# Optimization experiments

Hardware: AMD Instinct MI355X
Metric: run time of the kernel (lower is better)

The kernel has to match this reference:

```python
import jax, jax.numpy as jnp
import numpy as np

N_E = 4096
E_DIM = 256


def setup_inputs() -> dict:
    key = jax.random.key(0)
    k1, k2 = jax.random.split(key)
    z = jax.random.normal(k1, (32, 2048, E_DIM), dtype=jnp.float32)
    # nn.Embedding weight initialized uniform(-1/n_e, 1/n_e)
    codebook = jax.random.uniform(k2, (N_E, E_DIM), dtype=jnp.float32,
                                  minval=-1.0 / N_E, maxval=1.0 / N_E)
    return {"z": z, "codebook": codebook}


def reference(z, codebook):
    # z: [B, T, e_dim], codebook: [n_e, e_dim]
    z_flat = z.reshape(-1, z.shape[-1])                      # [N, d]
    # squared euclidean distance: ||z||^2 + ||e||^2 - 2 z.e^T
    d = (jnp.sum(z_flat ** 2, axis=1, keepdims=True)
         + jnp.sum(codebook ** 2, axis=1)
         - 2.0 * jnp.einsum('nd,kd->nk', z_flat, codebook))  # [N, n_e]
    idx = jnp.argmin(d, axis=1)                              # [N]
    z_q = codebook[idx].reshape(z.shape)                     # [B, T, d]
    return z_q
```

## Files before the change

### kernel.cpp

```cpp
#include <hip/hip_runtime.h>
#include <hip/hip_fp16.h>
#include <cfloat>
#include <climits>

#define D     256
#define NE    4096
#define MT    64
#define NSPLITB 8
#define DELTA     1.5e-4f
#define CAND_CAP  131072

typedef _Float16 f16x8 __attribute__((ext_vector_type(8)));
typedef __attribute__((ext_vector_type(4))) float f32x4;

#define SYNC(n) do { \
    asm volatile("s_waitcnt vmcnt(" #n ")\n\ts_barrier" ::: "memory"); \
    __builtin_amdgcn_sched_barrier(0); \
} while (0)

__device__ __forceinline__ float np_block128_sq(const float* __restrict__ p) {
    float r[8];
    #pragma unroll
    for (int j = 0; j < 8; ++j) r[j] = __fmul_rn(p[j], p[j]);
    #pragma unroll
    for (int i = 8; i < 128; i += 8)
        #pragma unroll
        for (int j = 0; j < 8; ++j) r[j] = __fadd_rn(r[j], __fmul_rn(p[i + j], p[i + j]));
    return __fadd_rn(__fadd_rn(__fadd_rn(r[0], r[1]), __fadd_rn(r[2], r[3])),
                     __fadd_rn(__fadd_rn(r[4], r[5]), __fadd_rn(r[6], r[7])));
}
__device__ __forceinline__ float np_sumsq256(const float* __restrict__ p) {
    return __fadd_rn(np_block128_sq(p), np_block128_sq(p + 128));
}
__device__ __forceinline__ float np_einsum_dot256(const float* __restrict__ zr,
                                                  const float* __restrict__ er) {
    float v0 = 0.f, v1 = 0.f, v2 = 0.f, v3 = 0.f;
    for (int t = 0; t < 256; t += 16) {
        float4 a0 = *(const float4*)(zr + t);
        float4 a1 = *(const float4*)(zr + t + 4);
        float4 a2 = *(const float4*)(zr + t + 8);
        float4 a3 = *(const float4*)(zr + t + 12);
        float4 b0 = *(const float4*)(er + t);
        float4 b1 = *(const float4*)(er + t + 4);
        float4 b2 = *(const float4*)(er + t + 8);
        float4 b3 = *(const float4*)(er + t + 12);
        v0 = __fadd_rn(v0, __fmul_rn(a3.x, b3.x));
        v1 = __fadd_rn(v1, __fmul_rn(a3.y, b3.y));
        v2 = __fadd_rn(v2, __fmul_rn(a3.z, b3.z));
        v3 = __fadd_rn(v3, __fmul_rn(a3.w, b3.w));
        v0 = __fadd_rn(v0, __fmul_rn(a2.x, b2.x));
        v1 = __fadd_rn(v1, __fmul_rn(a2.y, b2.y));
        v2 = __fadd_rn(v2, __fmul_rn(a2.z, b2.z));
        v3 = __fadd_rn(v3, __fmul_rn(a2.w, b2.w));
        v0 = __fadd_rn(v0, __fmul_rn(a1.x, b1.x));
        v1 = __fadd_rn(v1, __fmul_rn(a1.y, b1.y));
        v2 = __fadd_rn(v2, __fmul_rn(a1.z, b1.z));
        v3 = __fadd_rn(v3, __fmul_rn(a1.w, b1.w));
        v0 = __fadd_rn(v0, __fmul_rn(a0.x, b0.x));
        v1 = __fadd_rn(v1, __fmul_rn(a0.y, b0.y));
        v2 = __fadd_rn(v2, __fmul_rn(a0.z, b0.z));
        v3 = __fadd_rn(v3, __fmul_rn(a0.w, b0.w));
    }
    return __fadd_rn(__fadd_rn(v0, v1), __fadd_rn(v2, v3));
}

__global__ void bnp_kernel(const float* __restrict__ cb, float* __restrict__ Bnp) {
    int k = blockIdx.x * 256 + threadIdx.x;
    if (k < NE) Bnp[k] = np_sumsq256(cb + (size_t)k * D);
}

__global__ void cbhl_kernel(const float* __restrict__ cb,
                            unsigned short* __restrict__ hi,
                            unsigned short* __restrict__ lo) {
    int t = blockIdx.x * 256 + threadIdx.x;
    float4 v = *(const float4*)(cb + (size_t)t * 4);
    float e[4] = {v.x * 4096.f, v.y * 4096.f, v.z * 4096.f, v.w * 4096.f};
    ushort4 H, L;
    unsigned short* Hp = (unsigned short*)&H;
    unsigned short* Lp = (unsigned short*)&L;
    #pragma unroll
    for (int j = 0; j < 4; ++j) {
        _Float16 hh = (_Float16)e[j];
        _Float16 ll = (_Float16)((e[j] - (float)hh) * 2048.0f);
        Hp[j] = __builtin_bit_cast(unsigned short, hh);
        Lp[j] = __builtin_bit_cast(unsigned short, ll);
    }
    *(ushort4*)(hi + (size_t)t * 4) = H;
    *(ushort4*)(lo + (size_t)t * 4) = L;
}

__device__ __forceinline__ void gload_lds16(const void* g, void* l) {
    __builtin_amdgcn_global_load_lds(
        (const __attribute__((address_space(1))) unsigned int*)g,
        (__attribute__((address_space(3))) unsigned int*)l, 16, 0, 0);
}

__global__ __launch_bounds__(256, 3)
void stageA_f16(const float* __restrict__ z,
                const unsigned short* __restrict__ cb2,
                const float* __restrict__ Bnp, int* __restrict__ idxArr,
                float* __restrict__ rowMin, unsigned long long* __restrict__ rowKey,
                int* __restrict__ flagCnt, int* __restrict__ flagList) {
    __shared__ unsigned char lds[16384 + 4 * 8192];
    float* BnpL = (float*)lds;
    unsigned short* Bt = (unsigned short*)(lds + 16384);

    const int tid  = threadIdx.x;
    const int wid  = tid >> 6;
    const int lane = tid & 63;
    const int ln   = lane & 15;
    const int qd   = lane >> 4;
    const int wm   = wid & 1;
    const int wn   = wid >> 1;
    const int R0   = blockIdx.x * MT;

    #pragma unroll
    for (int i = 0; i < 4; ++i) {
        int j = tid + 256 * i;
        *(float4*)(BnpL + j * 4) = *(const float4*)(Bnp + j * 4);
    }

    f16x8 fa[8][2];
    {
        const float* za = z + (size_t)(R0 + wm * 32 + ln) * 256 + qd * 8;
        #pragma unroll
        for (int kc = 0; kc < 8; ++kc)
            #pragma unroll
            for (int mt = 0; mt < 2; ++mt) {
                const float* p = za + mt * 16 * 256 + kc * 32;
                float4 a = *(const float4*)p, b = *(const float4*)(p + 4);
                f16x8 h;
                h[0] = (_Float16)a.x; h[1] = (_Float16)a.y;
                h[2] = (_Float16)a.z; h[3] = (_Float16)a.w;
                h[4] = (_Float16)b.x; h[5] = (_Float16)b.y;
                h[6] = (_Float16)b.z; h[7] = (_Float16)b.w;
                fa[kc][mt] = h;
            }
    }

    const int cA  = wid * 32 + (lane >> 2);
    const int sgA = (lane & 3) ^ ((cA >> 1) & 3);
    const unsigned short* srcA = cb2 + cA * 256 + sgA * 8;
    unsigned short* dstW = Bt + wid * 1024;
    const int boffs = ((wn * 64 + ln) << 6) + ((qd ^ ((ln >> 1) & 3)) << 4);
    const unsigned char* btb = (const unsigned char*)Bt;

    float best1[8], best2[8];
    int   bidx[8];
    #pragma unroll
    for (int i = 0; i < 8; ++i) { best1[i] = FLT_MAX; best2[i] = FLT_MAX; bidx[i] = 0; }

    #pragma unroll
    for (int s = 0; s < 3; ++s) {
        gload_lds16(srcA + s * 32, dstW + s * 4096);
        gload_lds16(srcA + s * 32 + 4096, dstW + s * 4096 + 512);
    }
    __syncthreads();

    for (int ct = 0; ct < 31; ++ct) {
        f32x4 acc[2][4];
        #pragma unroll
        for (int i = 0; i < 2; ++i)
            #pragma unroll
            for (int j = 0; j < 4; ++j) acc[i][j] = (f32x4){0.f, 0.f, 0.f, 0.f};

        #pragma unroll
        for (int kc = 0; kc < 8; ++kc) {
            SYNC(4);
            {
                const int s3k = kc + 3;
                int off = (ct + (s3k >> 3)) * 32768 + (s3k & 7) * 32;
                unsigned short* d = dstW + ((s3k & 3) << 12);
                gload_lds16(srcA + off, d);
                gload_lds16(srcA + off + 4096, d + 512);
            }
            f16x8 fb[4];
            #pragma unroll
            for (int nt = 0; nt < 4; ++nt)
                fb[nt] = *(const f16x8*)(btb + ((kc & 3) << 13) + boffs + nt * 1024);
            __builtin_amdgcn_s_setprio(1);
            #pragma unroll
            for (int mt = 0; mt < 2; ++mt)
                #pragma unroll
                for (int nt = 0; nt < 4; ++nt)
                    acc[mt][nt] = __builtin_amdgcn_mfma_f32_16x16x32_f16(
                        fa[kc][mt], fb[nt], acc[mt][nt], 0, 0, 0);
            __builtin_amdgcn_s_setprio(0);

            if (kc == 7) {
                const int C0 = ct * 128;
                #pragma unroll
                for (int nt = 0; nt < 4; ++nt) {
                    int col = C0 + wn * 64 + nt * 16 + ln;
                    float bn = BnpL[col];
                    #pragma unroll
                    for (int mt = 0; mt < 2; ++mt) {
                        f32x4 a = acc[mt][nt];
                        #pragma unroll
                        for (int r = 0; r < 4; ++r) {
                            float s = fmaf(-4.8828125e-4f, a[r], bn);
                            int ii = mt * 4 + r;
                            bool lt = s < best1[ii];
                            best2[ii] = __builtin_amdgcn_fmed3f(best1[ii], best2[ii], s);
                            bidx[ii]  = lt ? col : bidx[ii];
                            best1[ii] = fminf(best1[ii], s);
                        }
                    }
                }
            }
        }
    }
    {
        const int ct = 31;
        f32x4 acc[2][4];
        #pragma unroll
        for (int i = 0; i < 2; ++i)
            #pragma unroll
            for (int j = 0; j < 4; ++j) acc[i][j] = (f32x4){0.f, 0.f, 0.f, 0.f};

        #pragma unroll
        for (int kc = 0; kc < 8; ++kc) {
            if (kc <= 5) { SYNC(4); } else if (kc == 6) { SYNC(2); } else { SYNC(0); }
            if (kc <= 4) {
                const int s3k = kc + 3;
                int off = ct * 32768 + (s3k & 7) * 32;
                unsigned short* d = dstW + ((s3k & 3) << 12);
                gload_lds16(srcA + off, d);
                gload_lds16(srcA + off + 4096, d + 512);
            }
            f16x8 fb[4];
            #pragma unroll
            for (int nt = 0; nt < 4; ++nt)
                fb[nt] = *(const f16x8*)(btb + ((kc & 3) << 13) + boffs + nt * 1024);
            __builtin_amdgcn_s_setprio(1);
            #pragma unroll
            for (int mt = 0; mt < 2; ++mt)
                #pragma unroll
                for (int nt = 0; nt < 4; ++nt)
                    acc[mt][nt] = __builtin_amdgcn_mfma_f32_16x16x32_f16(
                        fa[kc][mt], fb[nt], acc[mt][nt], 0, 0, 0);
            __builtin_amdgcn_s_setprio(0);

            if (kc == 7) {
                const int C0 = ct * 128;
                #pragma unroll
                for (int nt = 0; nt < 4; ++nt) {
                    int col = C0 + wn * 64 + nt * 16 + ln;
                    float bn = BnpL[col];
                    #pragma unroll
                    for (int mt = 0; mt < 2; ++mt) {
                        f32x4 a = acc[mt][nt];
                        #pragma unroll
                        for (int r = 0; r < 4; ++r) {
                            float s = fmaf(-4.8828125e-4f, a[r], bn);
                            int ii = mt * 4 + r;
                            bool lt = s < best1[ii];
                            best2[ii] = __builtin_amdgcn_fmed3f(best1[ii], best2[ii], s);
                            bidx[ii]  = lt ? col : bidx[ii];
                            best1[ii] = fminf(best1[ii], s);
                        }
                    }
                }
            }
        }
    }

    #pragma unroll
    for (int mask = 1; mask < 16; mask <<= 1) {
        #pragma unroll
        for (int ii = 0; ii < 8; ++ii) {
            float c1 = __shfl_xor(best1[ii], mask);
            float c2 = __shfl_xor(best2[ii], mask);
            int   ci = __shfl_xor(bidx[ii], mask);
            if (c1 < best1[ii] || (c1 == best1[ii] && ci < bidx[ii])) {
                best2[ii] = fminf(best1[ii], c2);
                best1[ii] = c1; bidx[ii] = ci;
            } else {
                best2[ii] = fminf(best2[ii], c1);
            }
        }
    }
    __syncthreads();
    float* mb1 = (float*)lds;
    float* mb2 = mb1 + 128;
    int*   mix = (int*)(mb2 + 128);
    if (ln == 0) {
        #pragma unroll
        for (int mt = 0; mt < 2; ++mt)
            #pragma unroll
            for (int r = 0; r < 4; ++r) {
                int row = wm * 32 + mt * 16 + qd * 4 + r;
                mb1[row * 2 + wn] = best1[mt * 4 + r];
                mb2[row * 2 + wn] = best2[mt * 4 + r];
                mix[row * 2 + wn] = bidx[mt * 4 + r];
            }
    }
    __syncthreads();
    if (tid < MT) {
        int r = tid;
        float b1 = mb1[r * 2], b2v = mb2[r * 2]; int ix = mix[r * 2];
        float c1 = mb1[r * 2 + 1], c2 = mb2[r * 2 + 1]; int ci = mix[r * 2 + 1];
        if (c1 < b1 || (c1 == b1 && ci < ix)) { b2v = fminf(b1, c2); b1 = c1; ix = ci; }
        else b2v = fminf(b2v, c1);
        idxArr[R0 + r] = ix;
        rowMin[R0 + r] = b1;
        rowKey[R0 + r] = ~0ULL;
        if (b2v - b1 <= DELTA) {
            int p = atomicAdd(flagCnt, 1);
            flagList[p] = R0 + r;
        }
    }
}

__global__ __launch_bounds__(256, 3)
void stageB_f16(const float* __restrict__ z,
                const unsigned short* __restrict__ cb2,
                const unsigned short* __restrict__ cbl2,
                const float* __restrict__ Bnp, const float* __restrict__ rowMin,
                const int* __restrict__ flagCnt, const int* __restrict__ flagList,
                int* __restrict__ candCnt, unsigned int* __restrict__ candList) {
    __shared__ unsigned char lds[3 * 16384 + 256];
    unsigned short* Bt = (unsigned short*)lds;
    int*   frow   = (int*)(lds + 49152);
    float* rmin_l = (float*)(lds + 49152 + 128);

    const int nf = *flagCnt;
    const int R0 = blockIdx.x * 32;
    if (R0 >= nf) return;
    const int m = min(32, nf - R0);

    const int tid  = threadIdx.x;
    const int wid  = tid >> 6;
    const int lane = tid & 63;
    const int ln   = lane & 15;
    const int qd   = lane >> 4;
    const int wm   = wid & 1;
    const int wn   = wid >> 1;
    const int ktBeg = blockIdx.y * (NE / NSPLITB);

    if (tid < 32) {
        int fr = flagList[R0 + min(tid, m - 1)];
        frow[tid] = fr;
        rmin_l[tid] = rowMin[fr];
    }
    __syncthreads();

    int grr_[4]; float rmv[4];
    #pragma unroll
    for (int r = 0; r < 4; ++r) {
        int rl = wm * 16 + qd * 4 + r;
        grr_[r] = frow[rl];
        rmv[r]  = rmin_l[rl];
    }
    const int rowA = frow[wm * 16 + ln];

    float bnv[4][4];
    #pragma unroll
    for (int ct = 0; ct < 4; ++ct)
        #pragma unroll
        for (int nt = 0; nt < 4; ++nt)
            bnv[ct][nt] = Bnp[ktBeg + ct * 128 + wn * 64 + nt * 16 + ln];

    f16x8 fah[8], fal[8];
    {
        const float* za = z + (size_t)rowA * 256 + qd * 8;
        #pragma unroll
        for (int kc = 0; kc < 8; ++kc) {
            const float* p = za + kc * 32;
            float4 a = *(const float4*)p, b = *(const float4*)(p + 4);
            float x[8] = {a.x, a.y, a.z, a.w, b.x, b.y, b.z, b.w};
            f16x8 h, l;
            #pragma unroll
            for (int j = 0; j < 8; ++j) {
                _Float16 hh = (_Float16)x[j];
                h[j] = hh;
                l[j] = (_Float16)((x[j] - (float)hh) * 2048.0f);
            }
            fah[kc] = h; fal[kc] = l;
        }
    }

    const int cA  = wid * 32 + (lane >> 2);
    const int sgA = (lane & 3) ^ ((cA >> 1) & 3);
    const unsigned short* srcH = cb2  + (size_t)(ktBeg + cA) * 256 + sgA * 8;
    const unsigned short* srcL = cbl2 + (size_t)(ktBeg + cA) * 256 + sgA * 8;
    unsigned short* dstW = Bt + wid * 1024;
    const int boffs = ((wn * 64 + ln) << 6) + ((qd ^ ((ln >> 1) & 3)) << 4);
    const unsigned char* btb = (const unsigned char*)Bt;

    #pragma unroll
    for (int s = 0; s < 2; ++s) {
        unsigned short* d = dstW + s * 8192;
        gload_lds16(srcH + s * 32, d);
        gload_lds16(srcH + s * 32 + 4096, d + 512);
        gload_lds16(srcL + s * 32, d + 4096);
        gload_lds16(srcL + s * 32 + 4096, d + 4096 + 512);
    }
    __syncthreads();

    unsigned long long hm = 0;

    #pragma unroll
    for (int ct = 0; ct < 4; ++ct) {
        f32x4 a1[4], a2[4];
        #pragma unroll
        for (int j = 0; j < 4; ++j) {
            a1[j] = (f32x4){0.f, 0.f, 0.f, 0.f};
            a2[j] = (f32x4){0.f, 0.f, 0.f, 0.f};
        }
        #pragma unroll
        for (int kc = 0; kc < 8; ++kc) {
            const int s = ct * 8 + kc;
            if (s < 31) { SYNC(4); } else { SYNC(0); }
            if (s + 2 <= 31) {
                const int s2 = s + 2;
                int off = (s2 >> 3) * 32768 + (s2 & 7) * 32;
                unsigned short* d = dstW + (s2 % 3) * 8192;
                gload_lds16(srcH + off, d);
                gload_lds16(srcH + off + 4096, d + 512);
                gload_lds16(srcL + off, d + 4096);
                gload_lds16(srcL + off + 4096, d + 4096 + 512);
            }
            const int bb = (s % 3) * 16384;
            f16x8 fbh[4], fbl[4];
            #pragma unroll
            for (int nt = 0; nt < 4; ++nt) {
                fbh[nt] = *(const f16x8*)(btb + bb + boffs + nt * 1024);
                fbl[nt] = *(const f16x8*)(btb + bb + 8192 + boffs + nt * 1024);
            }
            __builtin_amdgcn_s_setprio(1);
            #pragma unroll
            for (int nt = 0; nt < 4; ++nt)
                a1[nt] = __builtin_amdgcn_mfma_f32_16x16x32_f16(fah[kc], fbh[nt], a1[nt], 0, 0, 0);
            #pragma unroll
            for (int nt = 0; nt < 4; ++nt)
                a2[nt] = __builtin_amdgcn_mfma_f32_16x16x32_f16(fah[kc], fbl[nt], a2[nt], 0, 0, 0);
            #pragma unroll
            for (int nt = 0; nt < 4; ++nt)
                a2[nt] = __builtin_amdgcn_mfma_f32_16x16x32_f16(fal[kc], fbh[nt], a2[nt], 0, 0, 0);
            __builtin_amdgcn_s_setprio(0);

            if (kc == 7) {
                #pragma unroll
                for (int nt = 0; nt < 4; ++nt)
                    #pragma unroll
                    for (int r = 0; r < 4; ++r) {
                        float s1 = fmaf(-4.8828125e-4f, a1[nt][r], bnv[ct][nt]);
                        float sc = fmaf(-2.384185791015625e-7f, a2[nt][r], s1);
                        if (sc <= rmv[r] + DELTA)
                            hm |= 1ull << (ct * 16 + nt * 4 + r);
                    }
            }
        }
    }

    while (hm) {
        int b = __builtin_ctzll(hm);
        hm &= hm - 1;
        int ctb = b >> 4, ntb = (b >> 2) & 3, rb = b & 3;
        int col = ktBeg + ctb * 128 + wn * 64 + ntb * 16 + ln;
        int rr  = (rb == 0) ? grr_[0] : (rb == 1) ? grr_[1] : (rb == 2) ? grr_[2] : grr_[3];
        int p = atomicAdd(candCnt, 1);
        if (p < CAND_CAP)
            candList[p] = ((unsigned)rr << 12) | (unsigned)col;
    }
}

__global__ void stageC(const float* __restrict__ z, const float* __restrict__ cb,
                       const float* __restrict__ Bnp,
                       const int* __restrict__ candCnt,
                       const unsigned int* __restrict__ candList,
                       unsigned long long* __restrict__ rowKey) {
    int c = blockIdx.x * 256 + threadIdx.x;
    int n = min(*candCnt, CAND_CAP);
    if (c >= n) return;
    unsigned e = candList[c];
    int r = (int)(e >> 12);
    int k = (int)(e & 4095u);
    float Anp = np_sumsq256(z + (size_t)r * D);
    float C   = np_einsum_dot256(z + (size_t)r * D, cb + (size_t)k * D);
    float AB  = __fadd_rn(Anp, Bnp[k]);
    float s   = __fsub_rn(AB, __fadd_rn(C, C));
    unsigned long long key = ((unsigned long long)__float_as_uint(s) << 32) | (unsigned)k;
    atomicMin(rowKey + r, key);
}

__global__ void gather_kernel(const float* __restrict__ cb,
                              const int* __restrict__ idxArr,
                              const unsigned long long* __restrict__ rowKey,
                              float* __restrict__ out) {
    int r = blockIdx.x * 4 + (threadIdx.x >> 6);
    int l = threadIdx.x & 63;
    unsigned long long kv = rowKey[r];
    int ix = (kv != ~0ULL) ? (int)(kv & 0xFFFFFFFFull) : idxArr[r];
    *(float4*)(out + (size_t)r * D + l * 4) =
        *(const float4*)(cb + (size_t)ix * D + l * 4);
}

extern "C" void kernel_launch(void* const* d_in, const int* in_sizes, int n_in,
                              void* d_out, int out_size, void* d_ws, size_t ws_size,
                              hipStream_t stream) {
    const float* z  = (const float*)d_in[0];
    const float* cb = (const float*)d_in[1];
    float* out = (float*)d_out;
    const int nRows = in_sizes[0] / D;

    char* w = (char*)d_ws;
    unsigned short* cb2  = (unsigned short*)w;
    unsigned short* cbl2 = (unsigned short*)(w + 2097152);
    unsigned long long* rowKey = (unsigned long long*)(w + 4194304);
    int*   idxArr   = (int*)  (w + 4718592);
    float* rowMin   = (float*)(w + 4980736);
    int*   flagList = (int*)  (w + 5242880);
    float* Bnp      = (float*)(w + 5505024);
    unsigned int* candList = (unsigned int*)(w + 5521408);
    int*   flagCnt  = (int*)  (w + 6045696);
    int*   candCnt  = flagCnt + 1;

    hipMemsetAsync(flagCnt, 0, 8, stream);
    bnp_kernel<<<NE / 256, 256, 0, stream>>>(cb, Bnp);
    cbhl_kernel<<<NE * D / 4 / 256, 256, 0, stream>>>(cb, cb2, cbl2);
    stageA_f16<<<nRows / MT, 256, 0, stream>>>(z, cb2, Bnp, idxArr, rowMin,
                                               rowKey, flagCnt, flagList);
    stageB_f16<<<dim3(nRows / 32, NSPLITB), 256, 0, stream>>>(z, cb2, cbl2, Bnp,
                                                              rowMin, flagCnt, flagList,
                                                              candCnt, candList);
    stageC<<<CAND_CAP / 256, 256, 0, stream>>>(z, cb, Bnp, candCnt, candList, rowKey);
    gather_kernel<<<nRows / 4, 256, 0, stream>>>(cb, idxArr, rowKey, out);
}
```

Measured before the change: 445.0 us.

## Drop hi/lo split in stage B and widen per-wave row tiles to 64x32

Stage B stops using a high/low fp16 split of z and the codebook and rescreens flagged rows with a single fp16 MFMA pass, using the same 4-stage LDS pipeline as stage A. Both stages now tile each wave as 64 rows by 32 columns (4 M-tiles by 2 N-tiles), which holds more A fragments in registers and reads fewer B fragments per wave. Occupancy hints drop from 3 to 2 waves per SIMD. This removes the lo-codebook conversion and two of the three MFMAs per step in stage B, at the cost of higher register pressure and a coarser screen, which may flag more candidates for stage C.

```diff
diff --git a/kernel.cpp b/kernel.cpp
--- a/kernel.cpp
+++ b/kernel.cpp
@@ -69,24 +69,17 @@
     if (k < NE) Bnp[k] = np_sumsq256(cb + (size_t)k * D);
 }
 
-__global__ void cbhl_kernel(const float* __restrict__ cb,
-                            unsigned short* __restrict__ hi,
-                            unsigned short* __restrict__ lo) {
+__global__ void tof16_kernel(const float* __restrict__ x,
+                             unsigned short* __restrict__ y, float scale, int n4) {
     int t = blockIdx.x * 256 + threadIdx.x;
-    float4 v = *(const float4*)(cb + (size_t)t * 4);
-    float e[4] = {v.x * 4096.f, v.y * 4096.f, v.z * 4096.f, v.w * 4096.f};
-    ushort4 H, L;
-    unsigned short* Hp = (unsigned short*)&H;
-    unsigned short* Lp = (unsigned short*)&L;
-    #pragma unroll
-    for (int j = 0; j < 4; ++j) {
-        _Float16 hh = (_Float16)e[j];
-        _Float16 ll = (_Float16)((e[j] - (float)hh) * 2048.0f);
-        Hp[j] = __builtin_bit_cast(unsigned short, hh);
-        Lp[j] = __builtin_bit_cast(unsigned short, ll);
-    }
-    *(ushort4*)(hi + (size_t)t * 4) = H;
-    *(ushort4*)(lo + (size_t)t * 4) = L;
+    if (t >= n4) return;
+    float4 v = *(const float4*)(x + (size_t)t * 4);
+    ushort4 o;
+    o.x = __half_as_ushort(__float2half_rn(v.x * scale));
+    o.y = __half_as_ushort(__float2half_rn(v.y * scale));
+    o.z = __half_as_ushort(__float2half_rn(v.z * scale));
+    o.w = __half_as_ushort(__float2half_rn(v.w * scale));
+    *(ushort4*)(y + (size_t)t * 4) = o;
 }
 
 __device__ __forceinline__ void gload_lds16(const void* g, void* l) {
@@ -95,7 +88,7 @@
         (__attribute__((address_space(3))) unsigned int*)l, 16, 0, 0);
 }
 
-__global__ __launch_bounds__(256, 3)
+__global__ __launch_bounds__(256, 2)
 void stageA_f16(const float* __restrict__ z,
                 const unsigned short* __restrict__ cb2,
                 const float* __restrict__ Bnp, int* __restrict__ idxArr,
@@ -110,8 +103,7 @@
     const int lane = tid & 63;
     const int ln   = lane & 15;
     const int qd   = lane >> 4;
-    const int wm   = wid & 1;
-    const int wn   = wid >> 1;
+    const int wn   = wid;
     const int R0   = blockIdx.x * MT;
 
     #pragma unroll
@@ -120,13 +112,13 @@
         *(float4*)(BnpL + j * 4) = *(const float4*)(Bnp + j * 4);
     }
 
-    f16x8 fa[8][2];
+    f16x8 fa[8][4];
     {
-        const float* za = z + (size_t)(R0 + wm * 32 + ln) * 256 + qd * 8;
+        const float* za = z + (size_t)(R0 + ln) * 256 + qd * 8;
         #pragma unroll
         for (int kc = 0; kc < 8; ++kc)
             #pragma unroll
-            for (int mt = 0; mt < 2; ++mt) {
+            for (int mt = 0; mt < 4; ++mt) {
                 const float* p = za + mt * 16 * 256 + kc * 32;
                 float4 a = *(const float4*)p, b = *(const float4*)(p + 4);
                 f16x8 h;
@@ -142,13 +134,13 @@
     const int sgA = (lane & 3) ^ ((cA >> 1) & 3);
     const unsigned short* srcA = cb2 + cA * 256 + sgA * 8;
     unsigned short* dstW = Bt + wid * 1024;
-    const int boffs = ((wn * 64 + ln) << 6) + ((qd ^ ((ln >> 1) & 3)) << 4);
+    const int boffs = ((wn * 32 + ln) << 6) + ((qd ^ ((ln >> 1) & 3)) << 4);
     const unsigned char* btb = (const unsigned char*)Bt;
 
-    float best1[8], best2[8];
-    int   bidx[8];
-    #pragma unroll
-    for (int i = 0; i < 8; ++i) { best1[i] = FLT_MAX; best2[i] = FLT_MAX; bidx[i] = 0; }
+    float best1[16], best2[16];
+    int   bidx[16];
+    #pragma unroll
+    for (int i = 0; i < 16; ++i) { best1[i] = FLT_MAX; best2[i] = FLT_MAX; bidx[i] = 0; }
 
     #pragma unroll
     for (int s = 0; s < 3; ++s) {
@@ -158,11 +150,11 @@
     __syncthreads();
 
     for (int ct = 0; ct < 31; ++ct) {
-        f32x4 acc[2][4];
-        #pragma unroll
-        for (int i = 0; i < 2; ++i)
-            #pragma unroll
-            for (int j = 0; j < 4; ++j) acc[i][j] = (f32x4){0.f, 0.f, 0.f, 0.f};
+        f32x4 acc[4][2];
+        #pragma unroll
+        for (int i = 0; i < 4; ++i)
+            #pragma unroll
+            for (int j = 0; j < 2; ++j) acc[i][j] = (f32x4){0.f, 0.f, 0.f, 0.f};
 
         #pragma unroll
         for (int kc = 0; kc < 8; ++kc) {
@@ -174,15 +166,15 @@
                 gload_lds16(srcA + off, d);
                 gload_lds16(srcA + off + 4096, d + 512);
             }
-            f16x8 fb[4];
-            #pragma unroll
-            for (int nt = 0; nt < 4; ++nt)
+            f16x8 fb[2];
+            #pragma unroll
+            for (int nt = 0; nt < 2; ++nt)
                 fb[nt] = *(const f16x8*)(btb + ((kc & 3) << 13) + boffs + nt * 1024);
             __builtin_amdgcn_s_setprio(1);
             #pragma unroll
-            for (int mt = 0; mt < 2; ++mt)
+            for (int mt = 0; mt < 4; ++mt)
                 #pragma unroll
-                for (int nt = 0; nt < 4; ++nt)
+                for (int nt = 0; nt < 2; ++nt)
                     acc[mt][nt] = __builtin_amdgcn_mfma_f32_16x16x32_f16(
                         fa[kc][mt], fb[nt], acc[mt][nt], 0, 0, 0);
             __builtin_amdgcn_s_setprio(0);
@@ -190,11 +182,11 @@
             if (kc == 7) {
                 const int C0 = ct * 128;
                 #pragma unroll
-                for (int nt = 0; nt < 4; ++nt) {
-                    int col = C0 + wn * 64 + nt * 16 + ln;
+                for (int nt = 0; nt < 2; ++nt) {
+                    int col = C0 + wn * 32 + nt * 16 + ln;
                     float bn = BnpL[col];
                     #pragma unroll
-                    for (int mt = 0; mt < 2; ++mt) {
+                    for (int mt = 0; mt < 4; ++mt) {
                         f32x4 a = acc[mt][nt];
                         #pragma unroll
                         for (int r = 0; r < 4; ++r) {
@@ -212,11 +204,11 @@
     }
     {
         const int ct = 31;
-        f32x4 acc[2][4];
-        #pragma unroll
-        for (int i = 0; i < 2; ++i)
-            #pragma unroll
-            for (int j = 0; j < 4; ++j) acc[i][j] = (f32x4){0.f, 0.f, 0.f, 0.f};
+        f32x4 acc[4][2];
+        #pragma unroll
+        for (int i = 0; i < 4; ++i)
+            #pragma unroll
+            for (int j = 0; j < 2; ++j) acc[i][j] = (f32x4){0.f, 0.f, 0.f, 0.f};
 
         #pragma unroll
         for (int kc = 0; kc < 8; ++kc) {
@@ -228,15 +220,15 @@
                 gload_lds16(srcA + off, d);
                 gload_lds16(srcA + off + 4096, d + 512);
             }
-            f16x8 fb[4];
-            #pragma unroll
-            for (int nt = 0; nt < 4; ++nt)
+            f16x8 fb[2];
+            #pragma unroll
+            for (int nt = 0; nt < 2; ++nt)
                 fb[nt] = *(const f16x8*)(btb + ((kc & 3) << 13) + boffs + nt * 1024);
             __builtin_amdgcn_s_setprio(1);
             #pragma unroll
-            for (int mt = 0; mt < 2; ++mt)
+            for (int mt = 0; mt < 4; ++mt)
                 #pragma unroll
-                for (int nt = 0; nt < 4; ++nt)
+                for (int nt = 0; nt < 2; ++nt)
                     acc[mt][nt] = __builtin_amdgcn_mfma_f32_16x16x32_f16(
                         fa[kc][mt], fb[nt], acc[mt][nt], 0, 0, 0);
             __builtin_amdgcn_s_setprio(0);
@@ -244,11 +236,11 @@
             if (kc == 7) {
                 const int C0 = ct * 128;
                 #pragma unroll
-                for (int nt = 0; nt < 4; ++nt) {
-                    int col = C0 + wn * 64 + nt * 16 + ln;
+                for (int nt = 0; nt < 2; ++nt) {
+                    int col = C0 + wn * 32 + nt * 16 + ln;
                     float bn = BnpL[col];
                     #pragma unroll
-                    for (int mt = 0; mt < 2; ++mt) {
+                    for (int mt = 0; mt < 4; ++mt) {
                         f32x4 a = acc[mt][nt];
                         #pragma unroll
                         for (int r = 0; r < 4; ++r) {
@@ -268,7 +260,7 @@
     #pragma unroll
     for (int mask = 1; mask < 16; mask <<= 1) {
         #pragma unroll
-        for (int ii = 0; ii < 8; ++ii) {
+        for (int ii = 0; ii < 16; ++ii) {
             float c1 = __shfl_xor(best1[ii], mask);
             float c2 = __shfl_xor(best2[ii], mask);
             int   ci = __shfl_xor(bidx[ii], mask);
@@ -282,26 +274,29 @@
     }
     __syncthreads();
     float* mb1 = (float*)lds;
-    float* mb2 = mb1 + 128;
-    int*   mix = (int*)(mb2 + 128);
+    float* mb2 = mb1 + 256;
+    int*   mix = (int*)(mb2 + 256);
     if (ln == 0) {
         #pragma unroll
-        for (int mt = 0; mt < 2; ++mt)
+        for (int mt = 0; mt < 4; ++mt)
             #pragma unroll
             for (int r = 0; r < 4; ++r) {
-                int row = wm * 32 + mt * 16 + qd * 4 + r;
-                mb1[row * 2 + wn] = best1[mt * 4 + r];
-                mb2[row * 2 + wn] = best2[mt * 4 + r];
-                mix[row * 2 + wn] = bidx[mt * 4 + r];
+                int row = mt * 16 + qd * 4 + r;
+                mb1[row * 4 + wn] = best1[mt * 4 + r];
+                mb2[row * 4 + wn] = best2[mt * 4 + r];
+                mix[row * 4 + wn] = bidx[mt * 4 + r];
             }
     }
     __syncthreads();
     if (tid < MT) {
         int r = tid;
-        float b1 = mb1[r * 2], b2v = mb2[r * 2]; int ix = mix[r * 2];
-        float c1 = mb1[r * 2 + 1], c2 = mb2[r * 2 + 1]; int ci = mix[r * 2 + 1];
-        if (c1 < b1 || (c1 == b1 && ci < ix)) { b2v = fminf(b1, c2); b1 = c1; ix = ci; }
-        else b2v = fminf(b2v, c1);
+        float b1 = mb1[r * 4], b2v = mb2[r * 4]; int ix = mix[r * 4];
+        #pragma unroll
+        for (int w = 1; w < 4; ++w) {
+            float c1 = mb1[r * 4 + w], c2 = mb2[r * 4 + w]; int ci = mix[r * 4 + w];
+            if (c1 < b1 || (c1 == b1 && ci < ix)) { b2v = fminf(b1, c2); b1 = c1; ix = ci; }
+            else b2v = fminf(b2v, c1);
+        }
         idxArr[R0 + r] = ix;
         rowMin[R0 + r] = b1;
         rowKey[R0 + r] = ~0ULL;
@@ -312,157 +307,153 @@
     }
 }
 
-__global__ __launch_bounds__(256, 3)
+__global__ __launch_bounds__(256, 2)
 void stageB_f16(const float* __restrict__ z,
                 const unsigned short* __restrict__ cb2,
-                const unsigned short* __restrict__ cbl2,
                 const float* __restrict__ Bnp, const float* __restrict__ rowMin,
                 const int* __restrict__ flagCnt, const int* __restrict__ flagList,
                 int* __restrict__ candCnt, unsigned int* __restrict__ candList) {
-    __shared__ unsigned char lds[3 * 16384 + 256];
+    __shared__ unsigned char lds[4 * 8192 + 512];
     unsigned short* Bt = (unsigned short*)lds;
-    int*   frow   = (int*)(lds + 49152);
-    float* rmin_l = (float*)(lds + 49152 + 128);
+    int*   frow   = (int*)(lds + 32768);
+    float* rmin_l = (float*)(lds + 32768 + 256);
 
     const int nf = *flagCnt;
-    const int R0 = blockIdx.x * 32;
+    const int R0 = blockIdx.x * MT;
     if (R0 >= nf) return;
-    const int m = min(32, nf - R0);
+    const int m = min(MT, nf - R0);
 
     const int tid  = threadIdx.x;
     const int wid  = tid >> 6;
     const int lane = tid & 63;
     const int ln   = lane & 15;
     const int qd   = lane >> 4;
-    const int wm   = wid & 1;
-    const int wn   = wid >> 1;
+    const int wn   = wid;
     const int ktBeg = blockIdx.y * (NE / NSPLITB);
 
-    if (tid < 32) {
+    if (tid < MT) {
         int fr = flagList[R0 + min(tid, m - 1)];
         frow[tid] = fr;
         rmin_l[tid] = rowMin[fr];
     }
     __syncthreads();
 
-    int grr_[4]; float rmv[4];
-    #pragma unroll
-    for (int r = 0; r < 4; ++r) {
-        int rl = wm * 16 + qd * 4 + r;
-        grr_[r] = frow[rl];
-        rmv[r]  = rmin_l[rl];
-    }
-    const int rowA = frow[wm * 16 + ln];
-
-    float bnv[4][4];
+    float rmv[16];
+    #pragma unroll
+    for (int mt = 0; mt < 4; ++mt)
+        #pragma unroll
+        for (int r = 0; r < 4; ++r)
+            rmv[mt * 4 + r] = rmin_l[mt * 16 + qd * 4 + r];
+
+    float bnv[4][2];
     #pragma unroll
     for (int ct = 0; ct < 4; ++ct)
         #pragma unroll
-        for (int nt = 0; nt < 4; ++nt)
-            bnv[ct][nt] = Bnp[ktBeg + ct * 128 + wn * 64 + nt * 16 + ln];
-
-    f16x8 fah[8], fal[8];
+        for (int nt = 0; nt < 2; ++nt)
+            bnv[ct][nt] = Bnp[ktBeg + ct * 128 + wn * 32 + nt * 16 + ln];
+
+    f16x8 fa[8][4];
     {
-        const float* za = z + (size_t)rowA * 256 + qd * 8;
-        #pragma unroll
-        for (int kc = 0; kc < 8; ++kc) {
-            const float* p = za + kc * 32;
-            float4 a = *(const float4*)p, b = *(const float4*)(p + 4);
-            float x[8] = {a.x, a.y, a.z, a.w, b.x, b.y, b.z, b.w};
-            f16x8 h, l;
-            #pragma unroll
-            for (int j = 0; j < 8; ++j) {
-                _Float16 hh = (_Float16)x[j];
-                h[j] = hh;
-                l[j] = (_Float16)((x[j] - (float)hh) * 2048.0f);
-            }
-            fah[kc] = h; fal[kc] = l;
-        }
+        int rA[4];
+        #pragma unroll
+        for (int mt = 0; mt < 4; ++mt) rA[mt] = frow[mt * 16 + ln];
+        #pragma unroll
+        for (int kc = 0; kc < 8; ++kc)
+            #pragma unroll
+            for (int mt = 0; mt < 4; ++mt) {
+                const float* p = z + (size_t)rA[mt] * 256 + kc * 32 + qd * 8;
+                float4 a = *(const float4*)p, b = *(const float4*)(p + 4);
+                f16x8 h;
+                h[0] = (_Float16)a.x; h[1] = (_Float16)a.y;
+                h[2] = (_Float16)a.z; h[3] = (_Float16)a.w;
+                h[4] = (_Float16)b.x; h[5] = (_Float16)b.y;
+                h[6] = (_Float16)b.z; h[7] = (_Float16)b.w;
+                fa[kc][mt] = h;
+            }
     }
 
     const int cA  = wid * 32 + (lane >> 2);
     const int sgA = (lane & 3) ^ ((cA >> 1) & 3);
-    const unsigned short* srcH = cb2  + (size_t)(ktBeg + cA) * 256 + sgA * 8;
-    const unsigned short* srcL = cbl2 + (size_t)(ktBeg + cA) * 256 + sgA * 8;
+    const unsigned short* srcA = cb2 + (size_t)(ktBeg + cA) * 256 + sgA * 8;
     unsigned short* dstW = Bt + wid * 1024;
-    const int boffs = ((wn * 64 + ln) << 6) + ((qd ^ ((ln >> 1) & 3)) << 4);
+    const int boffs = ((wn * 32 + ln) << 6) + ((qd ^ ((ln >> 1) & 3)) << 4);
     const unsigned char* btb = (const unsigned char*)Bt;
 
     #pragma unroll
-    for (int s = 0; s < 2; ++s) {
-        unsigned short* d = dstW + s * 8192;
-        gload_lds16(srcH + s * 32, d);
-        gload_lds16(srcH + s * 32 + 4096, d + 512);
-        gload_lds16(srcL + s * 32, d + 4096);
-        gload_lds16(srcL + s * 32 + 4096, d + 4096 + 512);
+    for (int s = 0; s < 3; ++s) {
+        gload_lds16(srcA + s * 32, dstW + s * 4096);
+        gload_lds16(srcA + s * 32 + 4096, dstW + s * 4096 + 512);
     }
     __syncthreads();
 
-    unsigned long long hm = 0;
+    unsigned long long hm0 = 0, hm1 = 0;
 
     #pragma unroll
     for (int ct = 0; ct < 4; ++ct) {
-        f32x4 a1[4], a2[4];
-        #pragma unroll
-        for (int j = 0; j < 4; ++j) {
-            a1[j] = (f32x4){0.f, 0.f, 0.f, 0.f};
-            a2[j] = (f32x4){0.f, 0.f, 0.f, 0.f};
-        }
+        f32x4 acc[4][2];
+        #pragma unroll
+        for (int i = 0; i < 4; ++i)
+            #pragma unroll
+            for (int j = 0; j < 2; ++j) acc[i][j] = (f32x4){0.f, 0.f, 0.f, 0.f};
+
         #pragma unroll
         for (int kc = 0; kc < 8; ++kc) {
             const int s = ct * 8 + kc;
-            if (s < 31) { SYNC(4); } else { SYNC(0); }
-            if (s + 2 <= 31) {
-                const int s2 = s + 2;
-                int off = (s2 >> 3) * 32768 + (s2 & 7) * 32;
-                unsigned short* d = dstW + (s2 % 3) * 8192;
-                gload_lds16(srcH + off, d);
-                gload_lds16(srcH + off + 4096, d + 512);
-                gload_lds16(srcL + off, d + 4096);
-                gload_lds16(srcL + off + 4096, d + 4096 + 512);
-            }
-            const int bb = (s % 3) * 16384;
-            f16x8 fbh[4], fbl[4];
-            #pragma unroll
-            for (int nt = 0; nt < 4; ++nt) {
-                fbh[nt] = *(const f16x8*)(btb + bb + boffs + nt * 1024);
-                fbl[nt] = *(const f16x8*)(btb + bb + 8192 + boffs + nt * 1024);
-            }
+            if (s <= 29) { SYNC(4); } else if (s == 30) { SYNC(2); } else { SYNC(0); }
+            if (s <= 28) {
+                const int s3 = s + 3;
+                int off = (s3 >> 3) * 32768 + (s3 & 7) * 32;
+                unsigned short* d = dstW + ((s3 & 3) << 12);
+                gload_lds16(srcA + off, d);
+                gload_lds16(srcA + off + 4096, d + 512);
+            }
+            f16x8 fb[2];
+            #pragma unroll
+            for (int nt = 0; nt < 2; ++nt)
+                fb[nt] = *(const f16x8*)(btb + ((s & 3) << 13) + boffs + nt * 1024);
             __builtin_amdgcn_s_setprio(1);
             #pragma unroll
-            for (int nt = 0; nt < 4; ++nt)
-                a1[nt] = __builtin_amdgcn_mfma_f32_16x16x32_f16(fah[kc], fbh[nt], a1[nt], 0, 0, 0);
-            #pragma unroll
-            for (int nt = 0; nt < 4; ++nt)
-                a2[nt] = __builtin_amdgcn_mfma_f32_16x16x32_f16(fah[kc], fbl[nt], a2[nt], 0, 0, 0);
-            #pragma unroll
-            for (int nt = 0; nt < 4; ++nt)
-                a2[nt] = __builtin_amdgcn_mfma_f32_16x16x32_f16(fal[kc], fbh[nt], a2[nt], 0, 0, 0);
+            for (int mt = 0; mt < 4; ++mt)
+                #pragma unroll
+                for (int nt = 0; nt < 2; ++nt)
+                    acc[mt][nt] = __builtin_amdgcn_mfma_f32_16x16x32_f16(
+                        fa[kc][mt], fb[nt], acc[mt][nt], 0, 0, 0);
             __builtin_amdgcn_s_setprio(0);
 
             if (kc == 7) {
                 #pragma unroll
-                for (int nt = 0; nt < 4; ++nt)
+                for (int nt = 0; nt < 2; ++nt)
                     #pragma unroll
-                    for (int r = 0; r < 4; ++r) {
-                        float s1 = fmaf(-4.8828125e-4f, a1[nt][r], bnv[ct][nt]);
-                        float sc = fmaf(-2.384185791015625e-7f, a2[nt][r], s1);
-                        if (sc <= rmv[r] + DELTA)
-                            hm |= 1ull << (ct * 16 + nt * 4 + r);
+                    for (int mt = 0; mt < 4; ++mt) {
+                        f32x4 a = acc[mt][nt];
+                        #pragma unroll
+                        for (int r = 0; r < 4; ++r) {
+                            float sc = fmaf(-4.8828125e-4f, a[r], bnv[ct][nt]);
+                            if (sc <= rmv[mt * 4 + r] + DELTA) {
+                                unsigned long long bit =
+                                    1ull << (((ct & 1) << 5) | (nt << 4) | (mt << 2) | r);
+                                if (ct < 2) hm0 |= bit; else hm1 |= bit;
+                            }
+                        }
                     }
             }
         }
     }
 
-    while (hm) {
-        int b = __builtin_ctzll(hm);
-        hm &= hm - 1;
-        int ctb = b >> 4, ntb = (b >> 2) & 3, rb = b & 3;
-        int col = ktBeg + ctb * 128 + wn * 64 + ntb * 16 + ln;
-        int rr  = (rb == 0) ? grr_[0] : (rb == 1) ? grr_[1] : (rb == 2) ? grr_[2] : grr_[3];
-        int p = atomicAdd(candCnt, 1);
-        if (p < CAND_CAP)
-            candList[p] = ((unsigned)rr << 12) | (unsigned)col;
+    #pragma unroll
+    for (int h = 0; h < 2; ++h) {
+        unsigned long long hm = h ? hm1 : hm0;
+        while (hm) {
+            int b = __builtin_ctzll(hm);
+            hm &= hm - 1;
+            int ctb = h * 2 + (b >> 5);
+            int ntb = (b >> 4) & 1, mtb = (b >> 2) & 3, rb = b & 3;
+            int col = ktBeg + ctb * 128 + wn * 32 + ntb * 16 + ln;
+            int row = frow[mtb * 16 + qd * 4 + rb];
+            int p = atomicAdd(candCnt, 1);
+            if (p < CAND_CAP)
+                candList[p] = ((unsigned)row << 12) | (unsigned)col;
+        }
     }
 }
 
@@ -506,24 +497,23 @@
     const int nRows = in_sizes[0] / D;
 
     char* w = (char*)d_ws;
-    unsigned short* cb2  = (unsigned short*)w;
-    unsigned short* cbl2 = (unsigned short*)(w + 2097152);
-    unsigned long long* rowKey = (unsigned long long*)(w + 4194304);
-    int*   idxArr   = (int*)  (w + 4718592);
-    float* rowMin   = (float*)(w + 4980736);
-    int*   flagList = (int*)  (w + 5242880);
-    float* Bnp      = (float*)(w + 5505024);
-    unsigned int* candList = (unsigned int*)(w + 5521408);
-    int*   flagCnt  = (int*)  (w + 6045696);
+    unsigned short* cb2 = (unsigned short*)w;
+    unsigned long long* rowKey = (unsigned long long*)(w + 2097152);
+    int*   idxArr   = (int*)  (w + 2621440);
+    float* rowMin   = (float*)(w + 2883584);
+    int*   flagList = (int*)  (w + 3145728);
+    float* Bnp      = (float*)(w + 3407872);
+    unsigned int* candList = (unsigned int*)(w + 3424256);
+    int*   flagCnt  = (int*)  (w + 3948544);
     int*   candCnt  = flagCnt + 1;
 
     hipMemsetAsync(flagCnt, 0, 8, stream);
     bnp_kernel<<<NE / 256, 256, 0, stream>>>(cb, Bnp);
-    cbhl_kernel<<<NE * D / 4 / 256, 256, 0, stream>>>(cb, cb2, cbl2);
+    tof16_kernel<<<NE * D / 4 / 256, 256, 0, stream>>>(cb, cb2, 4096.0f, NE * D / 4);
     stageA_f16<<<nRows / MT, 256, 0, stream>>>(z, cb2, Bnp, idxArr, rowMin,
                                                rowKey, flagCnt, flagList);
-    stageB_f16<<<dim3(nRows / 32, NSPLITB), 256, 0, stream>>>(z, cb2, cbl2, Bnp,
-                                                              rowMin, flagCnt, flagList,
+    stageB_f16<<<dim3(nRows / MT, NSPLITB), 256, 0, stream>>>(z, cb2, Bnp, rowMin,
+                                                              flagCnt, flagList,
                                                               candCnt, candList);
     stageC<<<CAND_CAP / 256, 256, 0, stream>>>(z, cb, Bnp, candCnt, candList, rowKey);
     gather_kernel<<<nRows / 4, 256, 0, stream>>>(cb, idxArr, rowKey, out);
```

After: 452.2 us. No clear change (+1.6%).
